# Performance work log

Hardware: AMD Instinct MI355X
Metric: run time of the kernel (lower is better)

Reference implementation:

```python
import jax, jax.numpy as jnp
import numpy as np

K, D = 512, 64


def setup_inputs() -> dict:
    key = jax.random.key(0)
    k1, k2 = jax.random.split(key)
    z_e_x = jax.random.normal(k1, (32, 4096, D), dtype=jnp.float32)
    # nn.Embedding weight initialized uniform(-1/K, 1/K)
    codebook = jax.random.uniform(k2, (K, D), dtype=jnp.float32,
                                  minval=-1.0 / K, maxval=1.0 / K)
    return {"z_e_x": z_e_x, "codebook": codebook}


def reference(z_e_x, codebook):
    # vq(): pairwise squared L2 distances to codebook, then argmin.
    d = z_e_x.shape[-1]
    flat = z_e_x.reshape(-1, d)                                   # [N, D]
    # ||z||^2 - 2 z.e + ||e||^2  (addmm form from original vq)
    dists = (jnp.sum(flat * flat, axis=1, keepdims=True)
             - 2.0 * flat @ codebook.T
             + jnp.sum(codebook * codebook, axis=1))              # [N, K]
    indices = jnp.argmin(dists, axis=1)                            # [N]
    # latents: indices reshaped to input shape minus feature dim
    return indices.reshape(z_e_x.shape[:-1])
```

## Files before the change

kernel.cpp:

```cpp
#include <hip/hip_runtime.h>
#include <math.h>

#define K_CODES 512
#define D_DIM   64
#define BM      256
#define NCHUNK  128
#define THREADS 256
#define LSTR    72
#define EPS_GAP 4e-5f

#define WS_CNT_OFF  2048
#define WS_EH_OFF   4096
#define WS_EL_OFF   77824
#define WS_LIST_OFF 151552

typedef __attribute__((ext_vector_type(8))) short short8v;
typedef __attribute__((ext_vector_type(4))) float f32x4;

__device__ __forceinline__ float np_sumsq64(const float* zarr) {
    float L[16];
#pragma unroll
    for (int j = 0; j < 16; ++j)
        L[j] = __fadd_rn(
            __fadd_rn(__fmul_rn(zarr[j],      zarr[j]),
                      __fmul_rn(zarr[j + 16], zarr[j + 16])),
            __fadd_rn(__fmul_rn(zarr[j + 32], zarr[j + 32]),
                      __fmul_rn(zarr[j + 48], zarr[j + 48])));
    float m[8];
#pragma unroll
    for (int j = 0; j < 8; ++j) m[j] = __fadd_rn(L[j], L[j + 8]);
    float n4[4];
#pragma unroll
    for (int j = 0; j < 4; ++j) n4[j] = __fadd_rn(m[j], m[j + 4]);
    return __fadd_rn(__fadd_rn(n4[0], n4[2]), __fadd_rn(n4[1], n4[3]));
}

__device__ __forceinline__ unsigned short f32_bf16_rne(float x) {
    unsigned int u = __float_as_uint(x);
    unsigned int r = (u + 0x7FFFu + ((u >> 16) & 1u)) >> 16;
    return (unsigned short)r;
}
__device__ __forceinline__ float bf16_f32(unsigned short h) {
    return __uint_as_float(((unsigned int)h) << 16);
}
__device__ __forceinline__ void split2(float x, unsigned short& h, unsigned short& l) {
    h = f32_bf16_rne(x);
    l = f32_bf16_rne(x - bf16_f32(h));
}

__global__ __launch_bounds__(256)
void vq_prep_kernel(const float* __restrict__ cb, float* __restrict__ ws,
                    int do_split) {
    int k = blockIdx.x * blockDim.x + threadIdx.x;
    if (k == 0) *reinterpret_cast<int*>((char*)ws + WS_CNT_OFF) = 0;
    if (k >= K_CODES) return;
    float e[D_DIM];
    const float4* p = reinterpret_cast<const float4*>(cb + (size_t)k * D_DIM);
#pragma unroll
    for (int i = 0; i < 16; ++i) {
        float4 v = p[i];
        e[4*i+0]=v.x; e[4*i+1]=v.y; e[4*i+2]=v.z; e[4*i+3]=v.w;
    }
    ws[k] = np_sumsq64(e);
    if (do_split) {
        unsigned short* eh = reinterpret_cast<unsigned short*>((char*)ws + WS_EH_OFF)
                             + (size_t)k * LSTR;
        unsigned short* el = reinterpret_cast<unsigned short*>((char*)ws + WS_EL_OFF)
                             + (size_t)k * LSTR;
#pragma unroll
        for (int i = 0; i < D_DIM; ++i) {
            unsigned short h, l;
            split2(e[i], h, l);
            eh[i] = h; el[i] = l;
        }
#pragma unroll
        for (int i = D_DIM; i < LSTR; ++i) { eh[i] = 0; el[i] = 0; }
    }
}

__global__ __launch_bounds__(256)
void vq_pass1_fast(const float* __restrict__ z,
                   const unsigned short* __restrict__ eh_g,
                   const unsigned short* __restrict__ el_g,
                   const float* __restrict__ norms, int* __restrict__ out,
                   int* __restrict__ cnt, int* __restrict__ list, int cap, int n) {
    __shared__ __align__(16) unsigned short ehS[2][NCHUNK * LSTR];
    __shared__ __align__(16) unsigned short elS[2][NCHUNK * LSTR];
    __shared__ float nrmL[2][NCHUNK];

    const int tid  = threadIdx.x;
    const int l    = tid & 63;
    const int w    = tid >> 6;
    const int j    = l >> 4;
    const int c16  = l & 15;
    const int base = blockIdx.x * BM;

    {
        const char* esrc = (const char*)eh_g;
        const char* lsrc = (const char*)el_g;
#pragma unroll
        for (int r2 = 0; r2 < 4; ++r2) {
            size_t off = ((size_t)tid + (size_t)r2 * 256) * 16;
            __builtin_amdgcn_global_load_lds(
                (const __attribute__((address_space(1))) void*)(esrc + off),
                (__attribute__((address_space(3))) void*)((char*)ehS[0] + off), 16, 0, 0);
            __builtin_amdgcn_global_load_lds(
                (const __attribute__((address_space(1))) void*)(lsrc + off),
                (__attribute__((address_space(3))) void*)((char*)elS[0] + off), 16, 0, 0);
        }
        if (tid < 128) {
            size_t off = 16384 + (size_t)tid * 16;
            __builtin_amdgcn_global_load_lds(
                (const __attribute__((address_space(1))) void*)(esrc + off),
                (__attribute__((address_space(3))) void*)((char*)ehS[0] + off), 16, 0, 0);
            __builtin_amdgcn_global_load_lds(
                (const __attribute__((address_space(1))) void*)(lsrc + off),
                (__attribute__((address_space(3))) void*)((char*)elS[0] + off), 16, 0, 0);
        }
        if (tid < NCHUNK / 4)
            reinterpret_cast<float4*>(nrmL[0])[tid] =
                reinterpret_cast<const float4*>(norms)[tid];
    }

    short8v bzh[4][2], bzl[4][2];
#pragma unroll
    for (int p = 0; p < 4; ++p) {
        int row = base + (4 * w + p) * 16 + c16;
        if (row >= n) row = n - 1;
        const float* zp = z + (size_t)row * D_DIM + j * 8;
#pragma unroll
        for (int h = 0; h < 2; ++h) {
            float4 v0 = *reinterpret_cast<const float4*>(zp + h * 32);
            float4 v1 = *reinterpret_cast<const float4*>(zp + h * 32 + 4);
            unsigned short hh[8], ll[8];
            split2(v0.x, hh[0], ll[0]); split2(v0.y, hh[1], ll[1]);
            split2(v0.z, hh[2], ll[2]); split2(v0.w, hh[3], ll[3]);
            split2(v1.x, hh[4], ll[4]); split2(v1.y, hh[5], ll[5]);
            split2(v1.z, hh[6], ll[6]); split2(v1.w, hh[7], ll[7]);
            short8v th, tl;
#pragma unroll
            for (int i = 0; i < 8; ++i) { th[i] = (short)hh[i]; tl[i] = (short)ll[i]; }
            bzh[p][h] = th; bzl[p][h] = tl;
        }
    }

    float m1[4] = {INFINITY, INFINITY, INFINITY, INFINITY};
    float m2[4] = {INFINITY, INFINITY, INFINITY, INFINITY};
    int   i1[4] = {0, 0, 0, 0};

    for (int c = 0; c < 4; ++c) {
        const int buf = c & 1;
        __syncthreads();

        if (c < 3) {
            const char* esrc = (const char*)eh_g + (size_t)(c + 1) * (NCHUNK * LSTR * 2);
            const char* lsrc = (const char*)el_g + (size_t)(c + 1) * (NCHUNK * LSTR * 2);
#pragma unroll
            for (int r2 = 0; r2 < 4; ++r2) {
                size_t off = ((size_t)tid + (size_t)r2 * 256) * 16;
                __builtin_amdgcn_global_load_lds(
                    (const __attribute__((address_space(1))) void*)(esrc + off),
                    (__attribute__((address_space(3))) void*)((char*)ehS[buf ^ 1] + off), 16, 0, 0);
                __builtin_amdgcn_global_load_lds(
                    (const __attribute__((address_space(1))) void*)(lsrc + off),
                    (__attribute__((address_space(3))) void*)((char*)elS[buf ^ 1] + off), 16, 0, 0);
            }
            if (tid < 128) {
                size_t off = 16384 + (size_t)tid * 16;
                __builtin_amdgcn_global_load_lds(
                    (const __attribute__((address_space(1))) void*)(esrc + off),
                    (__attribute__((address_space(3))) void*)((char*)ehS[buf ^ 1] + off), 16, 0, 0);
                __builtin_amdgcn_global_load_lds(
                    (const __attribute__((address_space(1))) void*)(lsrc + off),
                    (__attribute__((address_space(3))) void*)((char*)elS[buf ^ 1] + off), 16, 0, 0);
            }
            if (tid < NCHUNK / 4)
                reinterpret_cast<float4*>(nrmL[buf ^ 1])[tid] =
                    reinterpret_cast<const float4*>(norms)[(c + 1) * (NCHUNK / 4) + tid];
        }

#pragma unroll
        for (int ct = 0; ct < 8; ++ct) {
            int ar = (ct * 16 + c16) * LSTR + j * 8;
            short8v aeh0 = *reinterpret_cast<const short8v*>(&ehS[buf][ar]);
            short8v aeh1 = *reinterpret_cast<const short8v*>(&ehS[buf][ar + 32]);
            short8v ael0 = *reinterpret_cast<const short8v*>(&elS[buf][ar]);
            short8v ael1 = *reinterpret_cast<const short8v*>(&elS[buf][ar + 32]);
            float4 nr = *reinterpret_cast<const float4*>(&nrmL[buf][ct * 16 + j * 4]);
            float nra[4] = {nr.x, nr.y, nr.z, nr.w};
            int kg0 = c * NCHUNK + ct * 16 + j * 4;
#pragma unroll
            for (int p = 0; p < 4; ++p) {
                f32x4 acc = {0.f, 0.f, 0.f, 0.f};
                acc = __builtin_amdgcn_mfma_f32_16x16x32_bf16(aeh0, bzh[p][0], acc, 0, 0, 0);
                acc = __builtin_amdgcn_mfma_f32_16x16x32_bf16(aeh1, bzh[p][1], acc, 0, 0, 0);
                acc = __builtin_amdgcn_mfma_f32_16x16x32_bf16(aeh0, bzl[p][0], acc, 0, 0, 0);
                acc = __builtin_amdgcn_mfma_f32_16x16x32_bf16(aeh1, bzl[p][1], acc, 0, 0, 0);
                acc = __builtin_amdgcn_mfma_f32_16x16x32_bf16(ael0, bzh[p][0], acc, 0, 0, 0);
                acc = __builtin_amdgcn_mfma_f32_16x16x32_bf16(ael1, bzh[p][1], acc, 0, 0, 0);
#pragma unroll
                for (int r = 0; r < 4; ++r) {
                    float s = fmaf(-2.0f, acc[r], nra[r]);
                    int kg = kg0 + r;
                    bool lt1 = s < m1[p];
                    float nm2 = lt1 ? m1[p] : fminf(s, m2[p]);
                    i1[p] = lt1 ? kg : i1[p];
                    m1[p] = lt1 ? s : m1[p];
                    m2[p] = nm2;
                }
            }
        }
    }

#pragma unroll
    for (int p = 0; p < 4; ++p) {
        float a1 = m1[p], a2 = m2[p]; int ai = i1[p];
#pragma unroll
        for (int off = 16; off <= 32; off <<= 1) {
            float o1 = __shfl_xor(a1, off, 64);
            float o2 = __shfl_xor(a2, off, 64);
            int   oi = __shfl_xor(ai, off, 64);
            float hi = fmaxf(a1, o1);
            bool take = o1 < a1;
            ai = take ? oi : ai;
            a1 = take ? o1 : a1;
            a2 = fminf(hi, fminf(a2, o2));
        }
        int  ptg    = base + (4 * w + p) * 16 + c16;
        bool writer = (j == 0) && (ptg < n);
        bool flag   = writer && (a2 - a1 <= EPS_GAP);
        unsigned long long m = __ballot(flag);
        int abase = 0;
        if (m) {
            int leader = __ffsll(m) - 1;
            if (l == leader) abase = atomicAdd(cnt, __popcll(m));
            abase = __shfl(abase, leader, 64);
        }
        if (writer) {
            int val = ai;
            if (flag) {
                int rank = __popcll(m & ((1ull << l) - 1ull));
                int slot = abase + rank;
                if (slot < cap) list[slot] = ptg;
                else            val |= (int)0x80000000;
            }
            out[ptg] = val;
        }
    }
}

__global__ __launch_bounds__(256)
void vq_pass1_legacy(const float* __restrict__ z, const float* __restrict__ cb,
                     const float* __restrict__ norms, int* __restrict__ out,
                     int* __restrict__ cnt, int* __restrict__ list, int cap, int n) {
    __shared__ unsigned short zhS[128 * LSTR];
    __shared__ unsigned short zlS[128 * LSTR];
    __shared__ unsigned short ehS[NCHUNK * LSTR];
    __shared__ unsigned short elS[NCHUNK * LSTR];
    __shared__ float nrmL[NCHUNK];

    const int tid  = threadIdx.x;
    const int l    = tid & 63;
    const int w    = tid >> 6;
    const int j    = l >> 4;
    const int c16  = l & 15;
    const int base = blockIdx.x * 128;

    const float4* z4 = reinterpret_cast<const float4*>(z);
#pragma unroll
    for (int rep = 0; rep < 8; ++rep) {
        int flat = rep * THREADS + tid;
        int pt   = flat >> 4;
        int dblk = flat & 15;
        int gp = base + pt; if (gp >= n) gp = n - 1;
        float4 v = z4[(size_t)gp * 16 + dblk];
        ushort4 h, lo;
        split2(v.x, h.x, lo.x); split2(v.y, h.y, lo.y);
        split2(v.z, h.z, lo.z); split2(v.w, h.w, lo.w);
        *reinterpret_cast<ushort4*>(&zhS[pt * LSTR + dblk * 4]) = h;
        *reinterpret_cast<ushort4*>(&zlS[pt * LSTR + dblk * 4]) = lo;
    }
    __syncthreads();

    short8v bzh[2][2], bzl[2][2];
#pragma unroll
    for (int p = 0; p < 2; ++p) {
        int pr = ((2 * w + p) * 16 + c16) * LSTR;
#pragma unroll
        for (int h = 0; h < 2; ++h) {
            int off = pr + h * 32 + j * 8;
            bzh[p][h] = *reinterpret_cast<const short8v*>(&zhS[off]);
            bzl[p][h] = *reinterpret_cast<const short8v*>(&zlS[off]);
        }
    }

    float m1[2] = {INFINITY, INFINITY};
    float m2[2] = {INFINITY, INFINITY};
    int   i1[2] = {0, 0};

    for (int c = 0; c < 4; ++c) {
        __syncthreads();
        const float4* cb4 = reinterpret_cast<const float4*>(cb);
#pragma unroll
        for (int rep = 0; rep < 8; ++rep) {
            int flat = rep * THREADS + tid;
            int code = flat >> 4;
            int dblk = flat & 15;
            float4 v = cb4[(size_t)(c * NCHUNK + code) * 16 + dblk];
            ushort4 h, lo;
            split2(v.x, h.x, lo.x); split2(v.y, h.y, lo.y);
            split2(v.z, h.z, lo.z); split2(v.w, h.w, lo.w);
            *reinterpret_cast<ushort4*>(&ehS[code * LSTR + dblk * 4]) = h;
            *reinterpret_cast<ushort4*>(&elS[code * LSTR + dblk * 4]) = lo;
        }
        if (tid < NCHUNK / 4)
            reinterpret_cast<float4*>(nrmL)[tid] =
                reinterpret_cast<const float4*>(norms)[c * (NCHUNK / 4) + tid];
        __syncthreads();

#pragma unroll
        for (int ct = 0; ct < 8; ++ct) {
            int ar = (ct * 16 + c16) * LSTR + j * 8;
            short8v aeh0 = *reinterpret_cast<const short8v*>(&ehS[ar]);
            short8v aeh1 = *reinterpret_cast<const short8v*>(&ehS[ar + 32]);
            short8v ael0 = *reinterpret_cast<const short8v*>(&elS[ar]);
            short8v ael1 = *reinterpret_cast<const short8v*>(&elS[ar + 32]);
            float4 nr = *reinterpret_cast<const float4*>(&nrmL[ct * 16 + j * 4]);
            float nra[4] = {nr.x, nr.y, nr.z, nr.w};
            int kg0 = c * NCHUNK + ct * 16 + j * 4;
#pragma unroll
            for (int p = 0; p < 2; ++p) {
                f32x4 acc = {0.f, 0.f, 0.f, 0.f};
                acc = __builtin_amdgcn_mfma_f32_16x16x32_bf16(aeh0, bzh[p][0], acc, 0, 0, 0);
                acc = __builtin_amdgcn_mfma_f32_16x16x32_bf16(aeh1, bzh[p][1], acc, 0, 0, 0);
                acc = __builtin_amdgcn_mfma_f32_16x16x32_bf16(aeh0, bzl[p][0], acc, 0, 0, 0);
                acc = __builtin_amdgcn_mfma_f32_16x16x32_bf16(aeh1, bzl[p][1], acc, 0, 0, 0);
                acc = __builtin_amdgcn_mfma_f32_16x16x32_bf16(ael0, bzh[p][0], acc, 0, 0, 0);
                acc = __builtin_amdgcn_mfma_f32_16x16x32_bf16(ael1, bzh[p][1], acc, 0, 0, 0);
#pragma unroll
                for (int r = 0; r < 4; ++r) {
                    float s = fmaf(-2.0f, acc[r], nra[r]);
                    int kg = kg0 + r;
                    bool lt1 = s < m1[p];
                    float nm2 = lt1 ? m1[p] : fminf(s, m2[p]);
                    i1[p] = lt1 ? kg : i1[p];
                    m1[p] = lt1 ? s : m1[p];
                    m2[p] = nm2;
                }
            }
        }
    }

#pragma unroll
    for (int p = 0; p < 2; ++p) {
        float a1 = m1[p], a2 = m2[p]; int ai = i1[p];
#pragma unroll
        for (int off = 16; off <= 32; off <<= 1) {
            float o1 = __shfl_xor(a1, off, 64);
            float o2 = __shfl_xor(a2, off, 64);
            int   oi = __shfl_xor(ai, off, 64);
            float hi = fmaxf(a1, o1);
            bool take = o1 < a1;
            ai = take ? oi : ai;
            a1 = take ? o1 : a1;
            a2 = fminf(hi, fminf(a2, o2));
        }
        int  ptg    = base + (2 * w + p) * 16 + c16;
        bool writer = (j == 0) && (ptg < n);
        bool flag   = writer && (a2 - a1 <= EPS_GAP);
        unsigned long long m = __ballot(flag);
        int abase = 0;
        if (m) {
            int leader = __ffsll(m) - 1;
            if (l == leader) abase = atomicAdd(cnt, __popcll(m));
            abase = __shfl(abase, leader, 64);
        }
        if (writer) {
            int val = ai;
            if (flag) {
                int rank = __popcll(m & ((1ull << l) - 1ull));
                int slot = abase + rank;
                if (slot < cap) list[slot] = ptg;
                else            val |= (int)0x80000000;
            }
            out[ptg] = val;
        }
    }
}

__device__ __forceinline__ void vq_rescan_point(
        const float* __restrict__ z, const float* __restrict__ cb,
        const float* __restrict__ norms, int* __restrict__ out,
        int pt, int lane) {
    float zr[D_DIM];
    const float4* zp = reinterpret_cast<const float4*>(z + (size_t)pt * D_DIM);
#pragma unroll
    for (int i = 0; i < 16; ++i) {
        float4 q = zp[i];
        zr[4*i+0]=q.x; zr[4*i+1]=q.y; zr[4*i+2]=q.z; zr[4*i+3]=q.w;
    }
    const float sz = np_sumsq64(zr);
    float best = INFINITY; int bi = 0x7FFFFFFF;
#pragma unroll 1
    for (int r = 0; r < 8; ++r) {
        const float4* e4 = reinterpret_cast<const float4*>(cb) +
                           ((size_t)(lane * 8 + r) << 4);
        float a = 0.f;
#pragma unroll
        for (int g = 0; g < 16; ++g) {
            float4 q = e4[g];
            a = fmaf(zr[4*g+0], q.x, a);
            a = fmaf(zr[4*g+1], q.y, a);
            a = fmaf(zr[4*g+2], q.z, a);
            a = fmaf(zr[4*g+3], q.w, a);
        }
        float s = __fadd_rn(__fsub_rn(sz, __fmul_rn(2.0f, a)),
                            norms[lane * 8 + r]);
        if (s < best) { best = s; bi = lane * 8 + r; }
    }
#pragma unroll
    for (int off = 1; off < 64; off <<= 1) {
        float os = __shfl_xor(best, off, 64);
        int   ok = __shfl_xor(bi, off, 64);
        if (os < best || (os == best && ok < bi)) { best = os; bi = ok; }
    }
    if (lane == 0) out[pt] = bi;
}

__global__ __launch_bounds__(256)
void vq_cleanup_kernel(const float* __restrict__ z, const float* __restrict__ cb,
                       const float* __restrict__ norms,
                       const int* __restrict__ cnt, const int* __restrict__ list,
                       int cap, int* __restrict__ out, int n) {
    const int lane   = threadIdx.x & 63;
    const int wid    = (blockIdx.x * blockDim.x + threadIdx.x) >> 6;
    const int nwaves = (gridDim.x * blockDim.x) >> 6;

    int total = *cnt;
    int lim   = total < cap ? total : cap;
    for (int i = wid; i < lim; i += nwaves)
        vq_rescan_point(z, cb, norms, out, list[i], lane);

    if (total > cap) {
        for (int b = wid * 64; b < n; b += nwaves * 64) {
            int t = b + lane;
            int v = (t < n) ? out[t] : 0;
            unsigned long long m = __ballot(v < 0);
            while (m) {
                int bb = __ffsll(m) - 1;
                m &= m - 1ull;
                vq_rescan_point(z, cb, norms, out, b + bb, lane);
            }
        }
    }
}

extern "C" void kernel_launch(void* const* d_in, const int* in_sizes, int n_in,
                              void* d_out, int out_size, void* d_ws, size_t ws_size,
                              hipStream_t stream) {
    const float* z  = (const float*)d_in[0];
    const float* cb = (const float*)d_in[1];
    int n = in_sizes[0] / D_DIM;
    float* norms = (float*)d_ws;
    int*   cnt   = (int*)((char*)d_ws + WS_CNT_OFF);
    int* out = (int*)d_out;

    bool fast = ws_size >= (size_t)WS_LIST_OFF + 4096;
    vq_prep_kernel<<<(K_CODES + 255) / 256, 256, 0, stream>>>(cb, norms, fast ? 1 : 0);

    if (fast) {
        const unsigned short* eh = (const unsigned short*)((char*)d_ws + WS_EH_OFF);
        const unsigned short* el = (const unsigned short*)((char*)d_ws + WS_EL_OFF);
        int* list = (int*)((char*)d_ws + WS_LIST_OFF);
        int  cap  = (int)((ws_size - WS_LIST_OFF) / 4);
        vq_pass1_fast<<<(n + BM - 1) / BM, THREADS, 0, stream>>>(
            z, eh, el, norms, out, cnt, list, cap, n);
        vq_cleanup_kernel<<<512, 256, 0, stream>>>(z, cb, norms, cnt, list, cap, out, n);
    } else {
        int* list = (int*)d_ws + 513;
        int  cap  = (int)(ws_size / 4) - 513; if (cap < 0) cap = 0;
        vq_pass1_legacy<<<(n + 127) / 128, THREADS, 0, stream>>>(
            z, cb, norms, out, cnt, list, cap, n);
        vq_cleanup_kernel<<<512, 256, 0, stream>>>(z, cb, norms, cnt, list, cap, out, n);
    }
}
```

Baseline: 66.08 us.

## Split codebook across two blocks per row tile and merge top-2 in separate kernel

The pass-1 kernel now handles half the codebook (256 codes) per block and launches twice as many blocks, writing per-half best/second-best distances and indices to workspace. A new merge kernel combines the two halves, applies the ambiguity gap test, and appends points to the rescan list. The intent is more parallelism and less LDS per block (single buffer), which may raise occupancy. The costs are redundant z loads and splits, an extra kernel launch, extra global traffic for the intermediate results, and loss of the double-buffered prefetch.

```diff
diff --git a/kernel.cpp b/kernel.cpp
--- a/kernel.cpp
+++ b/kernel.cpp
@@ -12,7 +12,7 @@
 #define WS_CNT_OFF  2048
 #define WS_EH_OFF   4096
 #define WS_EL_OFF   77824
-#define WS_LIST_OFF 151552
+#define WS_TRIP_OFF 151552
 
 typedef __attribute__((ext_vector_type(8))) short short8v;
 typedef __attribute__((ext_vector_type(4))) float f32x4;
@@ -79,47 +79,48 @@
 }
 
 __global__ __launch_bounds__(256)
-void vq_pass1_fast(const float* __restrict__ z,
-                   const unsigned short* __restrict__ eh_g,
-                   const unsigned short* __restrict__ el_g,
-                   const float* __restrict__ norms, int* __restrict__ out,
-                   int* __restrict__ cnt, int* __restrict__ list, int cap, int n) {
-    __shared__ __align__(16) unsigned short ehS[2][NCHUNK * LSTR];
-    __shared__ __align__(16) unsigned short elS[2][NCHUNK * LSTR];
-    __shared__ float nrmL[2][NCHUNK];
+void vq_pass1_ksplit(const float* __restrict__ z,
+                     const unsigned short* __restrict__ eh_g,
+                     const unsigned short* __restrict__ el_g,
+                     const float* __restrict__ norms,
+                     float2* __restrict__ trip, int* __restrict__ i1g, int n) {
+    __shared__ __align__(16) unsigned short ehS[NCHUNK * LSTR];
+    __shared__ __align__(16) unsigned short elS[NCHUNK * LSTR];
+    __shared__ float nrmL[NCHUNK];
 
     const int tid  = threadIdx.x;
     const int l    = tid & 63;
     const int w    = tid >> 6;
     const int j    = l >> 4;
     const int c16  = l & 15;
-    const int base = blockIdx.x * BM;
+    const int half = blockIdx.x & 1;
+    const int base = (blockIdx.x >> 1) * BM;
 
     {
-        const char* esrc = (const char*)eh_g;
-        const char* lsrc = (const char*)el_g;
+        const char* esrc = (const char*)eh_g + (size_t)(half * 2) * (NCHUNK * LSTR * 2);
+        const char* lsrc = (const char*)el_g + (size_t)(half * 2) * (NCHUNK * LSTR * 2);
 #pragma unroll
         for (int r2 = 0; r2 < 4; ++r2) {
             size_t off = ((size_t)tid + (size_t)r2 * 256) * 16;
             __builtin_amdgcn_global_load_lds(
                 (const __attribute__((address_space(1))) void*)(esrc + off),
-                (__attribute__((address_space(3))) void*)((char*)ehS[0] + off), 16, 0, 0);
+                (__attribute__((address_space(3))) void*)((char*)ehS + off), 16, 0, 0);
             __builtin_amdgcn_global_load_lds(
                 (const __attribute__((address_space(1))) void*)(lsrc + off),
-                (__attribute__((address_space(3))) void*)((char*)elS[0] + off), 16, 0, 0);
+                (__attribute__((address_space(3))) void*)((char*)elS + off), 16, 0, 0);
         }
         if (tid < 128) {
             size_t off = 16384 + (size_t)tid * 16;
             __builtin_amdgcn_global_load_lds(
                 (const __attribute__((address_space(1))) void*)(esrc + off),
-                (__attribute__((address_space(3))) void*)((char*)ehS[0] + off), 16, 0, 0);
+                (__attribute__((address_space(3))) void*)((char*)ehS + off), 16, 0, 0);
             __builtin_amdgcn_global_load_lds(
                 (const __attribute__((address_space(1))) void*)(lsrc + off),
-                (__attribute__((address_space(3))) void*)((char*)elS[0] + off), 16, 0, 0);
+                (__attribute__((address_space(3))) void*)((char*)elS + off), 16, 0, 0);
         }
         if (tid < NCHUNK / 4)
-            reinterpret_cast<float4*>(nrmL[0])[tid] =
-                reinterpret_cast<const float4*>(norms)[tid];
+            reinterpret_cast<float4*>(nrmL)[tid] =
+                reinterpret_cast<const float4*>(norms)[(half * 2) * (NCHUNK / 4) + tid];
     }
 
     short8v bzh[4][2], bzl[4][2];
@@ -148,47 +149,46 @@
     float m2[4] = {INFINITY, INFINITY, INFINITY, INFINITY};
     int   i1[4] = {0, 0, 0, 0};
 
-    for (int c = 0; c < 4; ++c) {
-        const int buf = c & 1;
-        __syncthreads();
-
-        if (c < 3) {
-            const char* esrc = (const char*)eh_g + (size_t)(c + 1) * (NCHUNK * LSTR * 2);
-            const char* lsrc = (const char*)el_g + (size_t)(c + 1) * (NCHUNK * LSTR * 2);
+    for (int c = 0; c < 2; ++c) {
+        if (c > 0) {
+            __syncthreads();
+            const char* esrc = (const char*)eh_g + (size_t)(half * 2 + c) * (NCHUNK * LSTR * 2);
+            const char* lsrc = (const char*)el_g + (size_t)(half * 2 + c) * (NCHUNK * LSTR * 2);
 #pragma unroll
             for (int r2 = 0; r2 < 4; ++r2) {
                 size_t off = ((size_t)tid + (size_t)r2 * 256) * 16;
                 __builtin_amdgcn_global_load_lds(
                     (const __attribute__((address_space(1))) void*)(esrc + off),
-                    (__attribute__((address_space(3))) void*)((char*)ehS[buf ^ 1] + off), 16, 0, 0);
+                    (__attribute__((address_space(3))) void*)((char*)ehS + off), 16, 0, 0);
                 __builtin_amdgcn_global_load_lds(
                     (const __attribute__((address_space(1))) void*)(lsrc + off),
-                    (__attribute__((address_space(3))) void*)((char*)elS[buf ^ 1] + off), 16, 0, 0);
+                    (__attribute__((address_space(3))) void*)((char*)elS + off), 16, 0, 0);
             }
             if (tid < 128) {
                 size_t off = 16384 + (size_t)tid * 16;
                 __builtin_amdgcn_global_load_lds(
                     (const __attribute__((address_space(1))) void*)(esrc + off),
-                    (__attribute__((address_space(3))) void*)((char*)ehS[buf ^ 1] + off), 16, 0, 0);
+                    (__attribute__((address_space(3))) void*)((char*)ehS + off), 16, 0, 0);
                 __builtin_amdgcn_global_load_lds(
                     (const __attribute__((address_space(1))) void*)(lsrc + off),
-                    (__attribute__((address_space(3))) void*)((char*)elS[buf ^ 1] + off), 16, 0, 0);
+                    (__attribute__((address_space(3))) void*)((char*)elS + off), 16, 0, 0);
             }
             if (tid < NCHUNK / 4)
-                reinterpret_cast<float4*>(nrmL[buf ^ 1])[tid] =
-                    reinterpret_cast<const float4*>(norms)[(c + 1) * (NCHUNK / 4) + tid];
-        }
+                reinterpret_cast<float4*>(nrmL)[tid] =
+                    reinterpret_cast<const float4*>(norms)[(half * 2 + c) * (NCHUNK / 4) + tid];
+        }
+        __syncthreads();
 
 #pragma unroll
         for (int ct = 0; ct < 8; ++ct) {
             int ar = (ct * 16 + c16) * LSTR + j * 8;
-            short8v aeh0 = *reinterpret_cast<const short8v*>(&ehS[buf][ar]);
-            short8v aeh1 = *reinterpret_cast<const short8v*>(&ehS[buf][ar + 32]);
-            short8v ael0 = *reinterpret_cast<const short8v*>(&elS[buf][ar]);
-            short8v ael1 = *reinterpret_cast<const short8v*>(&elS[buf][ar + 32]);
-            float4 nr = *reinterpret_cast<const float4*>(&nrmL[buf][ct * 16 + j * 4]);
+            short8v aeh0 = *reinterpret_cast<const short8v*>(&ehS[ar]);
+            short8v aeh1 = *reinterpret_cast<const short8v*>(&ehS[ar + 32]);
+            short8v ael0 = *reinterpret_cast<const short8v*>(&elS[ar]);
+            short8v ael1 = *reinterpret_cast<const short8v*>(&elS[ar + 32]);
+            float4 nr = *reinterpret_cast<const float4*>(&nrmL[ct * 16 + j * 4]);
             float nra[4] = {nr.x, nr.y, nr.z, nr.w};
-            int kg0 = c * NCHUNK + ct * 16 + j * 4;
+            int kg0 = half * 256 + c * NCHUNK + ct * 16 + j * 4;
 #pragma unroll
             for (int p = 0; p < 4; ++p) {
                 f32x4 acc = {0.f, 0.f, 0.f, 0.f};
@@ -226,26 +226,49 @@
             a1 = take ? o1 : a1;
             a2 = fminf(hi, fminf(a2, o2));
         }
-        int  ptg    = base + (4 * w + p) * 16 + c16;
-        bool writer = (j == 0) && (ptg < n);
-        bool flag   = writer && (a2 - a1 <= EPS_GAP);
-        unsigned long long m = __ballot(flag);
-        int abase = 0;
-        if (m) {
-            int leader = __ffsll(m) - 1;
-            if (l == leader) abase = atomicAdd(cnt, __popcll(m));
-            abase = __shfl(abase, leader, 64);
-        }
-        if (writer) {
-            int val = ai;
-            if (flag) {
-                int rank = __popcll(m & ((1ull << l) - 1ull));
-                int slot = abase + rank;
-                if (slot < cap) list[slot] = ptg;
-                else            val |= (int)0x80000000;
-            }
-            out[ptg] = val;
-        }
+        int pt = base + (4 * w + p) * 16 + c16;
+        if (j == 0 && pt < n) {
+            trip[2 * pt + half] = make_float2(a1, a2);
+            i1g[2 * pt + half]  = ai;
+        }
+    }
+}
+
+__global__ __launch_bounds__(256)
+void vq_merge_kernel(const float2* __restrict__ trip, const int* __restrict__ i1g,
+                     int* __restrict__ out, int* __restrict__ cnt,
+                     int* __restrict__ list, int cap, int n) {
+    int t = blockIdx.x * 256 + threadIdx.x;
+    int lane = threadIdx.x & 63;
+    bool valid = (t < n);
+    float m1 = INFINITY, m2 = INFINITY; int ig = 0;
+    if (valid) {
+        float2 a = trip[2 * t + 0], b = trip[2 * t + 1];
+        int ia = i1g[2 * t + 0],   ib = i1g[2 * t + 1];
+        bool bwin = b.x < a.x;
+        m1 = bwin ? b.x : a.x;
+        ig = bwin ? ib  : ia;
+        float loser = bwin ? a.x : b.x;
+        float wm2   = bwin ? b.y : a.y;
+        m2 = fminf(loser, wm2);
+    }
+    bool flag = valid && (m2 - m1 <= EPS_GAP);
+    unsigned long long m = __ballot(flag);
+    int abase = 0;
+    if (m) {
+        int leader = __ffsll(m) - 1;
+        if (lane == leader) abase = atomicAdd(cnt, __popcll(m));
+        abase = __shfl(abase, leader, 64);
+    }
+    if (valid) {
+        int val = ig;
+        if (flag) {
+            int rank = __popcll(m & ((1ull << lane) - 1ull));
+            int slot = abase + rank;
+            if (slot < cap) list[slot] = t;
+            else            val |= (int)0x80000000;
+        }
+        out[t] = val;
     }
 }
 
@@ -465,16 +488,24 @@
     int*   cnt   = (int*)((char*)d_ws + WS_CNT_OFF);
     int* out = (int*)d_out;
 
-    bool fast = ws_size >= (size_t)WS_LIST_OFF + 4096;
+    size_t trip_bytes = (size_t)n * 16;
+    size_t i1_bytes   = (size_t)n * 8;
+    size_t i1_off     = WS_TRIP_OFF + trip_bytes;
+    size_t list_off   = i1_off + i1_bytes;
+    bool fast = ws_size >= list_off + 4096;
+
     vq_prep_kernel<<<(K_CODES + 255) / 256, 256, 0, stream>>>(cb, norms, fast ? 1 : 0);
 
     if (fast) {
         const unsigned short* eh = (const unsigned short*)((char*)d_ws + WS_EH_OFF);
         const unsigned short* el = (const unsigned short*)((char*)d_ws + WS_EL_OFF);
-        int* list = (int*)((char*)d_ws + WS_LIST_OFF);
-        int  cap  = (int)((ws_size - WS_LIST_OFF) / 4);
-        vq_pass1_fast<<<(n + BM - 1) / BM, THREADS, 0, stream>>>(
-            z, eh, el, norms, out, cnt, list, cap, n);
+        float2* trip = (float2*)((char*)d_ws + WS_TRIP_OFF);
+        int*    i1g  = (int*)((char*)d_ws + i1_off);
+        int*    list = (int*)((char*)d_ws + list_off);
+        int     cap  = (int)((ws_size - list_off) / 4);
+        int nblk = (n + BM - 1) / BM;
+        vq_pass1_ksplit<<<2 * nblk, THREADS, 0, stream>>>(z, eh, el, norms, trip, i1g, n);
+        vq_merge_kernel<<<(n + 255) / 256, 256, 0, stream>>>(trip, i1g, out, cnt, list, cap, n);
         vq_cleanup_kernel<<<512, 256, 0, stream>>>(z, cb, norms, cnt, list, cap, out, n);
     } else {
         int* list = (int*)d_ws + 513;
```

Result: slower. 76.23 us (+15.4%).

## Stream codebook bf16 split fragments from global/L2 instead of LDS double-buffering

Applied to the files above, without the earlier changes.

Removes the LDS double-buffered staging of the codebook hi/lo bf16 arrays and the per-chunk barriers in the fast pass, so each wave reads its MFMA A-fragments straight from global memory (the small codebook is expected to sit in L2/L1). This cuts LDS traffic and __syncthreads stalls and frees shared memory, which may allow higher occupancy. The cost is that every wave issues redundant global loads with higher latency, hidden only by the unroll-8 loop and other resident waves.

```diff
diff --git a/kernel.cpp b/kernel.cpp
--- a/kernel.cpp
+++ b/kernel.cpp
@@ -4,7 +4,6 @@
 #define K_CODES 512
 #define D_DIM   64
 #define BM      256
-#define NCHUNK  128
 #define THREADS 256
 #define LSTR    72
 #define EPS_GAP 4e-5f
@@ -79,48 +78,17 @@
 }
 
 __global__ __launch_bounds__(256)
-void vq_pass1_fast(const float* __restrict__ z,
-                   const unsigned short* __restrict__ eh_g,
-                   const unsigned short* __restrict__ el_g,
-                   const float* __restrict__ norms, int* __restrict__ out,
-                   int* __restrict__ cnt, int* __restrict__ list, int cap, int n) {
-    __shared__ __align__(16) unsigned short ehS[2][NCHUNK * LSTR];
-    __shared__ __align__(16) unsigned short elS[2][NCHUNK * LSTR];
-    __shared__ float nrmL[2][NCHUNK];
-
+void vq_pass1_stream(const float* __restrict__ z,
+                     const unsigned short* __restrict__ eh_g,
+                     const unsigned short* __restrict__ el_g,
+                     const float* __restrict__ norms, int* __restrict__ out,
+                     int* __restrict__ cnt, int* __restrict__ list, int cap, int n) {
     const int tid  = threadIdx.x;
     const int l    = tid & 63;
     const int w    = tid >> 6;
     const int j    = l >> 4;
     const int c16  = l & 15;
     const int base = blockIdx.x * BM;
-
-    {
-        const char* esrc = (const char*)eh_g;
-        const char* lsrc = (const char*)el_g;
-#pragma unroll
-        for (int r2 = 0; r2 < 4; ++r2) {
-            size_t off = ((size_t)tid + (size_t)r2 * 256) * 16;
-            __builtin_amdgcn_global_load_lds(
-                (const __attribute__((address_space(1))) void*)(esrc + off),
-                (__attribute__((address_space(3))) void*)((char*)ehS[0] + off), 16, 0, 0);
-            __builtin_amdgcn_global_load_lds(
-                (const __attribute__((address_space(1))) void*)(lsrc + off),
-                (__attribute__((address_space(3))) void*)((char*)elS[0] + off), 16, 0, 0);
-        }
-        if (tid < 128) {
-            size_t off = 16384 + (size_t)tid * 16;
-            __builtin_amdgcn_global_load_lds(
-                (const __attribute__((address_space(1))) void*)(esrc + off),
-                (__attribute__((address_space(3))) void*)((char*)ehS[0] + off), 16, 0, 0);
-            __builtin_amdgcn_global_load_lds(
-                (const __attribute__((address_space(1))) void*)(lsrc + off),
-                (__attribute__((address_space(3))) void*)((char*)elS[0] + off), 16, 0, 0);
-        }
-        if (tid < NCHUNK / 4)
-            reinterpret_cast<float4*>(nrmL[0])[tid] =
-                reinterpret_cast<const float4*>(norms)[tid];
-    }
 
     short8v bzh[4][2], bzl[4][2];
 #pragma unroll
@@ -148,66 +116,35 @@
     float m2[4] = {INFINITY, INFINITY, INFINITY, INFINITY};
     int   i1[4] = {0, 0, 0, 0};
 
-    for (int c = 0; c < 4; ++c) {
-        const int buf = c & 1;
-        __syncthreads();
-
-        if (c < 3) {
-            const char* esrc = (const char*)eh_g + (size_t)(c + 1) * (NCHUNK * LSTR * 2);
-            const char* lsrc = (const char*)el_g + (size_t)(c + 1) * (NCHUNK * LSTR * 2);
-#pragma unroll
-            for (int r2 = 0; r2 < 4; ++r2) {
-                size_t off = ((size_t)tid + (size_t)r2 * 256) * 16;
-                __builtin_amdgcn_global_load_lds(
-                    (const __attribute__((address_space(1))) void*)(esrc + off),
-                    (__attribute__((address_space(3))) void*)((char*)ehS[buf ^ 1] + off), 16, 0, 0);
-                __builtin_amdgcn_global_load_lds(
-                    (const __attribute__((address_space(1))) void*)(lsrc + off),
-                    (__attribute__((address_space(3))) void*)((char*)elS[buf ^ 1] + off), 16, 0, 0);
-            }
-            if (tid < 128) {
-                size_t off = 16384 + (size_t)tid * 16;
-                __builtin_amdgcn_global_load_lds(
-                    (const __attribute__((address_space(1))) void*)(esrc + off),
-                    (__attribute__((address_space(3))) void*)((char*)ehS[buf ^ 1] + off), 16, 0, 0);
-                __builtin_amdgcn_global_load_lds(
-                    (const __attribute__((address_space(1))) void*)(lsrc + off),
-                    (__attribute__((address_space(3))) void*)((char*)elS[buf ^ 1] + off), 16, 0, 0);
-            }
-            if (tid < NCHUNK / 4)
-                reinterpret_cast<float4*>(nrmL[buf ^ 1])[tid] =
-                    reinterpret_cast<const float4*>(norms)[(c + 1) * (NCHUNK / 4) + tid];
-        }
-
-#pragma unroll
-        for (int ct = 0; ct < 8; ++ct) {
-            int ar = (ct * 16 + c16) * LSTR + j * 8;
-            short8v aeh0 = *reinterpret_cast<const short8v*>(&ehS[buf][ar]);
-            short8v aeh1 = *reinterpret_cast<const short8v*>(&ehS[buf][ar + 32]);
-            short8v ael0 = *reinterpret_cast<const short8v*>(&elS[buf][ar]);
-            short8v ael1 = *reinterpret_cast<const short8v*>(&elS[buf][ar + 32]);
-            float4 nr = *reinterpret_cast<const float4*>(&nrmL[buf][ct * 16 + j * 4]);
-            float nra[4] = {nr.x, nr.y, nr.z, nr.w};
-            int kg0 = c * NCHUNK + ct * 16 + j * 4;
-#pragma unroll
-            for (int p = 0; p < 4; ++p) {
-                f32x4 acc = {0.f, 0.f, 0.f, 0.f};
-                acc = __builtin_amdgcn_mfma_f32_16x16x32_bf16(aeh0, bzh[p][0], acc, 0, 0, 0);
-                acc = __builtin_amdgcn_mfma_f32_16x16x32_bf16(aeh1, bzh[p][1], acc, 0, 0, 0);
-                acc = __builtin_amdgcn_mfma_f32_16x16x32_bf16(aeh0, bzl[p][0], acc, 0, 0, 0);
-                acc = __builtin_amdgcn_mfma_f32_16x16x32_bf16(aeh1, bzl[p][1], acc, 0, 0, 0);
-                acc = __builtin_amdgcn_mfma_f32_16x16x32_bf16(ael0, bzh[p][0], acc, 0, 0, 0);
-                acc = __builtin_amdgcn_mfma_f32_16x16x32_bf16(ael1, bzh[p][1], acc, 0, 0, 0);
-#pragma unroll
-                for (int r = 0; r < 4; ++r) {
-                    float s = fmaf(-2.0f, acc[r], nra[r]);
-                    int kg = kg0 + r;
-                    bool lt1 = s < m1[p];
-                    float nm2 = lt1 ? m1[p] : fminf(s, m2[p]);
-                    i1[p] = lt1 ? kg : i1[p];
-                    m1[p] = lt1 ? s : m1[p];
-                    m2[p] = nm2;
-                }
+#pragma unroll 8
+    for (int ct = 0; ct < 32; ++ct) {
+        const unsigned short* er = eh_g + (size_t)(ct * 16 + c16) * LSTR + j * 8;
+        const unsigned short* lr = el_g + (size_t)(ct * 16 + c16) * LSTR + j * 8;
+        short8v aeh0 = *reinterpret_cast<const short8v*>(er);
+        short8v aeh1 = *reinterpret_cast<const short8v*>(er + 32);
+        short8v ael0 = *reinterpret_cast<const short8v*>(lr);
+        short8v ael1 = *reinterpret_cast<const short8v*>(lr + 32);
+        float4 nr = *reinterpret_cast<const float4*>(norms + ct * 16 + j * 4);
+        float nra[4] = {nr.x, nr.y, nr.z, nr.w};
+        int kg0 = ct * 16 + j * 4;
+#pragma unroll
+        for (int p = 0; p < 4; ++p) {
+            f32x4 acc = {0.f, 0.f, 0.f, 0.f};
+            acc = __builtin_amdgcn_mfma_f32_16x16x32_bf16(aeh0, bzh[p][0], acc, 0, 0, 0);
+            acc = __builtin_amdgcn_mfma_f32_16x16x32_bf16(aeh1, bzh[p][1], acc, 0, 0, 0);
+            acc = __builtin_amdgcn_mfma_f32_16x16x32_bf16(aeh0, bzl[p][0], acc, 0, 0, 0);
+            acc = __builtin_amdgcn_mfma_f32_16x16x32_bf16(aeh1, bzl[p][1], acc, 0, 0, 0);
+            acc = __builtin_amdgcn_mfma_f32_16x16x32_bf16(ael0, bzh[p][0], acc, 0, 0, 0);
+            acc = __builtin_amdgcn_mfma_f32_16x16x32_bf16(ael1, bzh[p][1], acc, 0, 0, 0);
+#pragma unroll
+            for (int r = 0; r < 4; ++r) {
+                float s = fmaf(-2.0f, acc[r], nra[r]);
+                int kg = kg0 + r;
+                bool lt1 = s < m1[p];
+                float nm2 = lt1 ? m1[p] : fminf(s, m2[p]);
+                i1[p] = lt1 ? kg : i1[p];
+                m1[p] = lt1 ? s : m1[p];
+                m2[p] = nm2;
             }
         }
     }
@@ -255,9 +192,9 @@
                      int* __restrict__ cnt, int* __restrict__ list, int cap, int n) {
     __shared__ unsigned short zhS[128 * LSTR];
     __shared__ unsigned short zlS[128 * LSTR];
-    __shared__ unsigned short ehS[NCHUNK * LSTR];
-    __shared__ unsigned short elS[NCHUNK * LSTR];
-    __shared__ float nrmL[NCHUNK];
+    __shared__ unsigned short ehS[128 * LSTR];
+    __shared__ unsigned short elS[128 * LSTR];
+    __shared__ float nrmL[128];
 
     const int tid  = threadIdx.x;
     const int l    = tid & 63;
@@ -306,16 +243,16 @@
             int flat = rep * THREADS + tid;
             int code = flat >> 4;
             int dblk = flat & 15;
-            float4 v = cb4[(size_t)(c * NCHUNK + code) * 16 + dblk];
+            float4 v = cb4[(size_t)(c * 128 + code) * 16 + dblk];
             ushort4 h, lo;
             split2(v.x, h.x, lo.x); split2(v.y, h.y, lo.y);
             split2(v.z, h.z, lo.z); split2(v.w, h.w, lo.w);
             *reinterpret_cast<ushort4*>(&ehS[code * LSTR + dblk * 4]) = h;
             *reinterpret_cast<ushort4*>(&elS[code * LSTR + dblk * 4]) = lo;
         }
-        if (tid < NCHUNK / 4)
+        if (tid < 32)
             reinterpret_cast<float4*>(nrmL)[tid] =
-                reinterpret_cast<const float4*>(norms)[c * (NCHUNK / 4) + tid];
+                reinterpret_cast<const float4*>(norms)[c * 32 + tid];
         __syncthreads();
 
 #pragma unroll
@@ -327,7 +264,7 @@
             short8v ael1 = *reinterpret_cast<const short8v*>(&elS[ar + 32]);
             float4 nr = *reinterpret_cast<const float4*>(&nrmL[ct * 16 + j * 4]);
             float nra[4] = {nr.x, nr.y, nr.z, nr.w};
-            int kg0 = c * NCHUNK + ct * 16 + j * 4;
+            int kg0 = c * 128 + ct * 16 + j * 4;
 #pragma unroll
             for (int p = 0; p < 2; ++p) {
                 f32x4 acc = {0.f, 0.f, 0.f, 0.f};
@@ -473,7 +410,7 @@
         const unsigned short* el = (const unsigned short*)((char*)d_ws + WS_EL_OFF);
         int* list = (int*)((char*)d_ws + WS_LIST_OFF);
         int  cap  = (int)((ws_size - WS_LIST_OFF) / 4);
-        vq_pass1_fast<<<(n + BM - 1) / BM, THREADS, 0, stream>>>(
+        vq_pass1_stream<<<(n + BM - 1) / BM, THREADS, 0, stream>>>(
             z, eh, el, norms, out, cnt, list, cap, n);
         vq_cleanup_kernel<<<512, 256, 0, stream>>>(z, cb, norms, cnt, list, cap, out, n);
     } else {
```

New measurement: 75.49 us. 14.2% more time.
